# Optimization experiments

Measured on AMD Instinct MI355X. Metric: run time of the kernel, lower is better.

The kernel has to match this reference:

```python
import jax, jax.numpy as jnp
import numpy as np

B, C, T_IN, R, TB = 8192, 3, 2048, 64, 128
ALPHA = 10.0  # steepness of sigmoid surrogate spike
Q_INIT = 6.0


def surrogate_spike(x):
    # Differentiable surrogate for the spiking nonlinearity (sigmoid fast-spike).
    return jax.nn.sigmoid(ALPHA * x)


def setup_inputs() -> dict:
    key = jax.random.key(0)
    k0, k1 = jax.random.split(key)
    traces = jax.random.normal(k0, (B, C, T_IN), jnp.float32)
    drive_w = jax.random.normal(k1, (R, C), jnp.float32) / np.sqrt(C)
    drive_b = jnp.zeros((R,), jnp.float32)
    frequency_raw = jnp.linspace(-1.2, 1.2, R, dtype=jnp.float32)
    q_center = float(np.log(np.exp(max(Q_INIT - 1.5, 1e-3)) - 1.0))  # inverse softplus
    q_raw = jnp.full((R,), q_center, jnp.float32)
    threshold_raw = jnp.zeros((R,), jnp.float32)
    return dict(traces=traces, drive_w=drive_w, drive_b=drive_b,
                frequency_raw=frequency_raw, q_raw=q_raw, threshold_raw=threshold_raw)


def reference(traces, drive_w, drive_b, frequency_raw, q_raw, threshold_raw):
    b, c, t = traces.shape
    win = t // TB  # adaptive_avg_pool1d with evenly-dividing window
    pooled = traces.reshape(b, c, TB, win).mean(axis=-1)  # [B, C, TB]
    # _normalize_traces: divide by per-sample max-abs clamped to >= 1
    scale = jnp.maximum(jnp.max(jnp.abs(pooled), axis=(1, 2), keepdims=True), 1.0)
    pooled = pooled / scale
    # 1x1 Conv1d == per-timestep linear projection C -> R
    drive = jnp.einsum('bct,rc->brt', pooled, drive_w) + drive_b[None, :, None]  # [B, R, TB]

    frequency = 0.03 + 0.17 * jax.nn.sigmoid(frequency_raw)      # [R]
    q_factor = 1.5 + jax.nn.softplus(q_raw)                      # [R]
    decay = jnp.exp(-1.0 / q_factor)                             # [R]
    threshold = 0.35 + 0.75 * jax.nn.sigmoid(threshold_raw)      # [R]

    def step(carry, current):
        state, velocity = carry
        velocity = decay * velocity + current - frequency * state
        state = state + frequency * velocity
        spikes = surrogate_spike(state - threshold)
        state = state - spikes * threshold
        return (state, velocity), spikes

    init = (jnp.zeros((b, R), drive.dtype), jnp.zeros((b, R), drive.dtype))
    drive_t = jnp.moveaxis(drive, -1, 0)  # [TB, B, R]
    _, spike_seq = jax.lax.scan(step, init, drive_t)  # spike_seq: [TB, B, R]
    return spike_seq.mean(axis=0)  # [B, R]
```

## Files before the change

kernel.cpp:

```cpp
#include <hip/hip_runtime.h>
#include <math.h>

constexpr int kC   = 3;
constexpr int kTIn = 2048;
constexpr int kR   = 64;
constexpr int kTB  = 128;
constexpr float kAlpha = 10.0f;
constexpr float kLog2e = 1.44269504088896f;

constexpr int kK   = 4;
constexpr int kF4  = kC * kTIn / 4;

#ifndef __has_builtin
#define __has_builtin(x) 0
#endif

static __device__ __forceinline__ float fast_rcp(float x) {
#if __has_builtin(__builtin_amdgcn_rcpf)
    return __builtin_amdgcn_rcpf(x);
#else
    return 1.0f / x;
#endif
}

static __device__ __forceinline__ float fast_exp2(float x) {
#if __has_builtin(__builtin_amdgcn_exp2f)
    return __builtin_amdgcn_exp2f(x);
#else
    return __builtin_exp2f(x);
#endif
}

__global__ void param_kernel(const float* __restrict__ freq_raw,
                             const float* __restrict__ q_raw,
                             const float* __restrict__ thr_raw,
                             float* __restrict__ pp)
{
    const int r = threadIdx.x;
    if (r >= kR) return;
    const float freq  = 0.03f + 0.17f / (1.0f + expf(-freq_raw[r]));
    const float qf    = 1.5f + log1pf(expf(q_raw[r]));
    const float decay = expf(-1.0f / qf);
    const float thr   = 0.35f + 0.75f / (1.0f + expf(-thr_raw[r]));
    pp[0 * kR + r] = freq;
    pp[1 * kR + r] = decay;
    pp[2 * kR + r] = thr;
    pp[3 * kR + r] = thr * (kAlpha * kLog2e);
}

__global__ __launch_bounds__(256, 8)
void fused_encoder_kernel(const float* __restrict__ traces,
                          const float* __restrict__ drive_w,
                          const float* __restrict__ drive_b,
                          const float* __restrict__ pp,
                          float* __restrict__ out)
{
    __shared__ float sp[2][kTB * 4];
    __shared__ float red[2][3];

    const int tid  = threadIdx.x;
    const int wave = tid >> 6;
    const int lane = tid & 63;
    const int scanWave = blockIdx.x & 3;
    const long long base = (long long)blockIdx.x * kK;
    const float4* tr4 = reinterpret_cast<const float4*>(traces);

    if (wave != scanWave) {
        const int h = wave - (wave > scanWave ? 1 : 0);

        auto pool = [&](long long b, int buf) {
            const float4* src = tr4 + b * kF4 + (h * 8) * 64 + lane;
            float mloc = 0.0f;
            #pragma unroll
            for (int j = 0; j < 8; ++j) {
                float4 v = src[j * 64];
                float s = (v.x + v.y) + (v.z + v.w);
                s += __shfl_xor(s, 1, 64);
                s += __shfl_xor(s, 2, 64);
                mloc = fmaxf(mloc, fabsf(s));
                if ((lane & 3) == 0) {
                    int w = (h * 8 + j) * 16 + (lane >> 2);
                    sp[buf][(w & 127) * 4 + (w >> 7)] = s;
                }
            }
            #pragma unroll
            for (int off = 4; off <= 32; off <<= 1)
                mloc = fmaxf(mloc, __shfl_xor(mloc, off, 64));
            if (lane == 0) red[buf][h] = mloc;
        };

        pool(base, 0);
        __syncthreads();
        for (int k = 0; k < kK; ++k) {
            if (k + 1 < kK) pool(base + k + 1, (k + 1) & 1);
            __syncthreads();
        }
    } else {
        const int r = lane;
        const float w0   = drive_w[r * kC + 0];
        const float w1   = drive_w[r * kC + 1];
        const float w2   = drive_w[r * kC + 2];
        const float bias = drive_b[r];
        const float freq  = pp[0 * kR + r];
        const float decay = pp[1 * kR + r];
        const float thr   = pp[2 * kR + r];
        const float thrE  = pp[3 * kR + r];
        const float expScale = kAlpha * kLog2e;

        __syncthreads();
        for (int k = 0; k < kK; ++k) {
            const int cur = k & 1;
            const float mm = fmaxf(fmaxf(red[cur][0], red[cur][1]), red[cur][2]);
            const float inv = fast_rcp(fmaxf(mm * (1.0f / 16.0f), 1.0f)) * (1.0f / 16.0f);
            const float v0 = w0 * inv, v1 = w1 * inv, v2 = w2 * inv;
            const float4* pt = reinterpret_cast<const float4*>(sp[cur]);

            __builtin_amdgcn_s_setprio(1);
            float state = 0.0f, vel = 0.0f, acc = 0.0f;
            #pragma unroll 8
            for (int t = 0; t < kTB; ++t) {
                float4 p = pt[t];
                float cur_ = fmaf(p.x, v0, bias);
                cur_ = fmaf(p.y, v1, cur_);
                cur_ = fmaf(p.z, v2, cur_);
                vel = fmaf(decay, vel, cur_);
                vel = fmaf(-freq, state, vel);
                state = fmaf(freq, vel, state);
                float e = fast_exp2(fmaf(-expScale, state, thrE));
                float spike = fast_rcp(1.0f + e);
                state = fmaf(-spike, thr, state);
                acc += spike;
            }
            __builtin_amdgcn_s_setprio(0);

            out[(base + k) * kR + r] = acc * (1.0f / kTB);
            __syncthreads();
        }
    }
}

extern "C" void kernel_launch(void* const* d_in, const int* in_sizes, int n_in,
                              void* d_out, int out_size, void* d_ws, size_t ws_size,
                              hipStream_t stream)
{
    const float* traces   = (const float*)d_in[0];
    const float* drive_w  = (const float*)d_in[1];
    const float* drive_b  = (const float*)d_in[2];
    const float* freq_raw = (const float*)d_in[3];
    const float* q_raw    = (const float*)d_in[4];
    const float* thr_raw  = (const float*)d_in[5];
    float* out = (float*)d_out;
    float* pp  = (float*)d_ws;

    const int totalB = in_sizes[0] / (kC * kTIn);
    const int grid = totalB / kK;

    param_kernel<<<1, 64, 0, stream>>>(freq_raw, q_raw, thr_raw, pp);
    fused_encoder_kernel<<<grid, 256, 0, stream>>>(traces, drive_w, drive_b, pp, out);
}
```

Measured before the change: 44.35 us.

## Prefetch next batch traces into registers across lightweight custom barriers

```diff
diff --git a/kernel.cpp b/kernel.cpp
--- a/kernel.cpp
+++ b/kernel.cpp
@@ -29,6 +29,23 @@
 #else
     return __builtin_exp2f(x);
 #endif
+}
+
+static __device__ __forceinline__ void sched_pin() {
+#if __has_builtin(__builtin_amdgcn_sched_barrier)
+    __builtin_amdgcn_sched_barrier(0);
+#endif
+}
+
+static __device__ __forceinline__ void bar_publish() {
+    asm volatile("s_waitcnt lgkmcnt(0)" ::: "memory");
+    __builtin_amdgcn_s_barrier();
+    asm volatile("" ::: "memory");
+}
+static __device__ __forceinline__ void bar_wait() {
+    asm volatile("" ::: "memory");
+    __builtin_amdgcn_s_barrier();
+    asm volatile("" ::: "memory");
 }
 
 __global__ void param_kernel(const float* __restrict__ freq_raw,
@@ -68,12 +85,17 @@
     if (wave != scanWave) {
         const int h = wave - (wave > scanWave ? 1 : 0);
 
-        auto pool = [&](long long b, int buf) {
+        float4 R[8];
+        auto issue = [&](long long b) {
             const float4* src = tr4 + b * kF4 + (h * 8) * 64 + lane;
+            #pragma unroll
+            for (int j = 0; j < 8; ++j) R[j] = src[j * 64];
+        };
+        auto consume = [&](int buf) {
             float mloc = 0.0f;
             #pragma unroll
             for (int j = 0; j < 8; ++j) {
-                float4 v = src[j * 64];
+                float4 v = R[j];
                 float s = (v.x + v.y) + (v.z + v.w);
                 s += __shfl_xor(s, 1, 64);
                 s += __shfl_xor(s, 2, 64);
@@ -89,11 +111,16 @@
             if (lane == 0) red[buf][h] = mloc;
         };
 
-        pool(base, 0);
-        __syncthreads();
-        for (int k = 0; k < kK; ++k) {
-            if (k + 1 < kK) pool(base + k + 1, (k + 1) & 1);
-            __syncthreads();
+        issue(base + 0);
+        consume(0);
+        issue(base + 1);
+        sched_pin();
+        bar_publish();
+        for (int k = 0; k < kK - 1; ++k) {
+            consume((k + 1) & 1);
+            if (k + 2 < kK) issue(base + k + 2);
+            sched_pin();
+            bar_publish();
         }
     } else {
         const int r = lane;
@@ -107,7 +134,7 @@
         const float thrE  = pp[3 * kR + r];
         const float expScale = kAlpha * kLog2e;
 
-        __syncthreads();
+        bar_wait();
         for (int k = 0; k < kK; ++k) {
             const int cur = k & 1;
             const float mm = fmaxf(fmaxf(red[cur][0], red[cur][1]), red[cur][2]);
@@ -134,7 +161,7 @@
             __builtin_amdgcn_s_setprio(0);
 
             out[(base + k) * kR + r] = acc * (1.0f / kTB);
-            __syncthreads();
+            if (k < kK - 1) bar_wait();
         }
     }
 }
```

Result: slower. 53.35 us (+20.3%).
